# Optimization experiments

Hardware: AMD Instinct MI355X
Metric: run time of the kernel (lower is better)

## Reference

```python
import jax, jax.numpy as jnp
import numpy as np

B = 8192
L = 64
N = L * L          # 4096 lattice sites
H = 256            # hidden size
NL = 8             # coupling layers
NM = N // 2        # masked sites per layer (checkerboard, even L)


def _checkerboard_indices():
    ii, jj = np.meshgrid(np.arange(L), np.arange(L), indexing='ij')
    cb = ((ii + jj) % 2).reshape(-1)
    out = []
    for parity in (0, 1):
        m = np.where(cb == parity)[0].astype(np.int32)   # frozen sites
        u = np.where(cb != parity)[0].astype(np.int32)   # transformed sites
        out.append((jnp.asarray(m), jnp.asarray(u)))
    return out


def setup_inputs() -> dict:
    key = jax.random.key(0)
    ks = jax.random.split(key, 7)
    sc = 0.02  # keep MLP activations in a sane range (orig zero-inits last layer)
    return {
        'z':  jax.random.normal(ks[0], (B, N), dtype=jnp.float32),
        'W1': jax.random.normal(ks[1], (NL, NM, H), dtype=jnp.float32) * sc,
        'b1': jax.random.normal(ks[2], (NL, H), dtype=jnp.float32) * sc,
        'W2': jax.random.normal(ks[3], (NL, H, H), dtype=jnp.float32) * sc,
        'b2': jax.random.normal(ks[4], (NL, H), dtype=jnp.float32) * sc,
        'W3': jax.random.normal(ks[5], (NL, H, 2 * NM), dtype=jnp.float32) * sc,
        'b3': jax.random.normal(ks[6], (NL, 2 * NM), dtype=jnp.float32) * sc,
    }


def reference(z, W1, b1, W2, b2, W3, b3):
    idx = _checkerboard_indices()  # static constants
    x = z
    log_det = jnp.zeros(z.shape[0], dtype=z.dtype)
    for i in range(NL):
        im, iu = idx[i % 2]
        xm = x[:, im]                                        # (B, NM) gather of frozen half
        h = jax.nn.leaky_relu(xm @ W1[i] + b1[i], 0.2)        # (B, H)
        h = jax.nn.leaky_relu(h @ W2[i] + b2[i], 0.2)         # (B, H)
        st = h @ W3[i] + b3[i]                                # (B, 2*NM)
        s, t = jnp.split(st, 2, axis=1)
        s = 2.0 * jnp.tanh(s)
        x = x.at[:, iu].set(x[:, iu] * jnp.exp(s) + t)        # scatter affine-transformed half
        log_det = log_det + s.sum(axis=1)
    return x, log_det
```

## Files before the change

### kernel.cpp

```cpp
#include <hip/hip_runtime.h>
#include <stdint.h>

#define BATCH   8192
#define NTOT    4096
#define HID     256
#define NLAYERS 8
#define NMASK   2048
#define HALF    ((size_t)BATCH * NMASK)

typedef unsigned short ushort_t;
typedef float  f32x4  __attribute__((ext_vector_type(4)));
typedef __bf16 bf16x8 __attribute__((ext_vector_type(8)));
typedef unsigned short u16x4 __attribute__((ext_vector_type(4)));

__device__ __forceinline__ unsigned short f2bf(float f) {
    union { float f; unsigned u; } v; v.f = f;
    unsigned r = v.u + 0x7FFFu + ((v.u >> 16) & 1u);
    return (unsigned short)(r >> 16);
}
__device__ __forceinline__ float bf2f(unsigned short h) {
    union { float f; unsigned u; } v; v.u = ((unsigned)h) << 16;
    return v.f;
}
__device__ __forceinline__ void split2(float f, unsigned short& hi, unsigned short& lo) {
    hi = f2bf(f);
    lo = f2bf(f - bf2f(hi));
}
__device__ __forceinline__ void async16(const void* g, void* l) {
    __builtin_amdgcn_global_load_lds(
        (const __attribute__((address_space(1))) unsigned int*)g,
        (__attribute__((address_space(3))) unsigned int*)l, 16, 0, 0);
}

__global__ __launch_bounds__(256) void split_transpose_kernel(
    const float* __restrict__ W,
    ushort_t* __restrict__ Whi, ushort_t* __restrict__ Wlo,
    int K, int N)
{
    __shared__ float tile[32][33];
    const int l  = blockIdx.z;
    const int k0 = blockIdx.x * 32;
    const int n0 = blockIdx.y * 32;
    const float* Wl = W + (size_t)l * K * N;
    const int tx = threadIdx.x & 31;
    const int ty = threadIdx.x >> 5;
#pragma unroll
    for (int it = 0; it < 4; ++it) {
        int r = ty + it * 8;
        tile[r][tx] = Wl[(size_t)(k0 + r) * N + (n0 + tx)];
    }
    __syncthreads();
    const size_t obase = (size_t)l * N * K;
#pragma unroll
    for (int it = 0; it < 4; ++it) {
        int r = ty + it * 8;
        float v = tile[tx][r];
        unsigned short hi, lo; split2(v, hi, lo);
        size_t oi = obase + (size_t)(n0 + r) * K + (k0 + tx);
        Whi[oi] = hi; Wlo[oi] = lo;
    }
}

__global__ __launch_bounds__(256) void prep_split(
    const float* __restrict__ z,
    ushort_t* __restrict__ xsh, ushort_t* __restrict__ xsl)
{
    size_t f = (((size_t)blockIdx.x * 256) + threadIdx.x) * 4;
    int row = (int)(f >> 11);
    int n   = (int)(f & 2047);
    int sel = (n >> 5) & 1;
    const float4* zp = (const float4*)(z + (size_t)row * NTOT + 2 * (size_t)n);
    float4 z01 = zp[0], z23 = zp[1];
    float e[8] = {z01.x, z01.y, z01.z, z01.w, z23.x, z23.y, z23.z, z23.w};
    u16x4 ah, al, bh, bl;
#pragma unroll
    for (int i = 0; i < 4; ++i) {
        float c0 = e[2 * i], c1 = e[2 * i + 1];
        float a = sel ? c1 : c0;
        float b = sel ? c0 : c1;
        unsigned short h, l;
        split2(a, h, l); ah[i] = h; al[i] = l;
        split2(b, h, l); bh[i] = h; bl[i] = l;
    }
    size_t off = (size_t)row * NMASK + n;
    *(u16x4*)&xsh[off] = ah;        *(u16x4*)&xsl[off] = al;
    *(u16x4*)&xsh[HALF + off] = bh; *(u16x4*)&xsl[HALF + off] = bl;
}

__global__ __launch_bounds__(256) void finalize_x(
    const ushort_t* __restrict__ xsh, const ushort_t* __restrict__ xsl,
    float* __restrict__ xout)
{
    size_t f = (((size_t)blockIdx.x * 256) + threadIdx.x) * 4;
    int row = (int)(f >> 11);
    int n   = (int)(f & 2047);
    int sel = (n >> 5) & 1;
    size_t off = (size_t)row * NMASK + n;
    u16x4 ah = *(const u16x4*)&xsh[off],        al = *(const u16x4*)&xsl[off];
    u16x4 bh = *(const u16x4*)&xsh[HALF + off], bl = *(const u16x4*)&xsl[HALF + off];
    float o[8];
#pragma unroll
    for (int i = 0; i < 4; ++i) {
        float va = bf2f(ah[i]) + bf2f(al[i]);
        float vb = bf2f(bh[i]) + bf2f(bl[i]);
        o[2 * i]     = sel ? vb : va;
        o[2 * i + 1] = sel ? va : vb;
    }
    float* op = xout + (size_t)row * NTOT + 2 * (size_t)n;
    ((float4*)op)[0] = make_float4(o[0], o[1], o[2], o[3]);
    ((float4*)op)[1] = make_float4(o[4], o[5], o[6], o[7]);
}

template<int MODE>
__global__ __launch_bounds__(256) void gemm128(
    const ushort_t* __restrict__ Ahi, const ushort_t* __restrict__ Alo, int lda,
    const ushort_t* __restrict__ Bhi, const ushort_t* __restrict__ Blo, int ldb,
    int nk,
    float* __restrict__ Pout,
    const float* __restrict__ bias,
    ushort_t* __restrict__ Ohi, ushort_t* __restrict__ Olo)
{
    __shared__ __align__(16) ushort_t Ah[128 * 32], Al[128 * 32];
    __shared__ __align__(16) ushort_t Bh[128 * 32], Bl[128 * 32];

    const int t = threadIdx.x;
    const int row0 = blockIdx.x * 128;
    const int col0 = blockIdx.y * 128;
    const int k0   = blockIdx.z * nk * 32;
    const int w  = t >> 6, L = t & 63;
    const int q  = L >> 4, nl = L & 15;
    const int wr = w >> 1, wc = w & 1;

    f32x4 acc[4][4] = {};

    for (int kt = 0; kt < nk; ++kt) {
        const int kk = k0 + kt * 32;
#pragma unroll
        for (int pass = 0; pass < 2; ++pass) {
            const int chunk = t + pass * 256;
            const int r  = chunk >> 2;
            const int ko = (chunk & 3) * 8;
            async16(Ahi + (size_t)(row0 + r) * lda + kk + ko, (char*)Ah + chunk * 16);
            async16(Alo + (size_t)(row0 + r) * lda + kk + ko, (char*)Al + chunk * 16);
            async16(Bhi + (size_t)(col0 + r) * ldb + kk + ko, (char*)Bh + chunk * 16);
            async16(Blo + (size_t)(col0 + r) * ldb + kk + ko, (char*)Bl + chunk * 16);
        }
        __syncthreads();

        bf16x8 a_h[4], a_l[4];
#pragma unroll
        for (int mt = 0; mt < 4; ++mt) {
            const int r = wr * 64 + mt * 16 + nl;
            a_h[mt] = *(const bf16x8*)&Ah[r * 32 + q * 8];
            a_l[mt] = *(const bf16x8*)&Al[r * 32 + q * 8];
        }
#pragma unroll
        for (int nt = 0; nt < 4; ++nt) {
            const int c = wc * 64 + nt * 16 + nl;
            bf16x8 b_h = *(const bf16x8*)&Bh[c * 32 + q * 8];
            bf16x8 b_l = *(const bf16x8*)&Bl[c * 32 + q * 8];
#pragma unroll
            for (int mt = 0; mt < 4; ++mt) {
                acc[mt][nt] = __builtin_amdgcn_mfma_f32_16x16x32_bf16(a_h[mt], b_h, acc[mt][nt], 0, 0, 0);
                acc[mt][nt] = __builtin_amdgcn_mfma_f32_16x16x32_bf16(a_h[mt], b_l, acc[mt][nt], 0, 0, 0);
                acc[mt][nt] = __builtin_amdgcn_mfma_f32_16x16x32_bf16(a_l[mt], b_h, acc[mt][nt], 0, 0, 0);
            }
        }
        __syncthreads();
    }

    if (MODE == 0) {
        float* out = Pout + (size_t)blockIdx.z * BATCH * HID;
#pragma unroll
        for (int mt = 0; mt < 4; ++mt)
#pragma unroll
            for (int r = 0; r < 4; ++r) {
                const int row = row0 + wr * 64 + mt * 16 + q * 4 + r;
                float* op = out + (size_t)row * HID + col0 + wc * 64 + nl;
#pragma unroll
                for (int nt = 0; nt < 4; ++nt)
                    op[nt * 16] = acc[mt][nt][r];
            }
    } else {
#pragma unroll
        for (int mt = 0; mt < 4; ++mt)
#pragma unroll
            for (int nt = 0; nt < 4; ++nt) {
                const int col = col0 + wc * 64 + nt * 16 + nl;
                const float bv = bias[col];
#pragma unroll
                for (int r = 0; r < 4; ++r) {
                    const int row = row0 + wr * 64 + mt * 16 + q * 4 + r;
                    float v = acc[mt][nt][r] + bv;
                    v = v > 0.f ? v : 0.2f * v;
                    unsigned short hh, ll; split2(v, hh, ll);
                    Ohi[(size_t)row * HID + col] = hh;
                    Olo[(size_t)row * HID + col] = ll;
                }
            }
    }
}

__global__ __launch_bounds__(256) void combine_leaky(
    const float* __restrict__ P, const float* __restrict__ bias,
    ushort_t* __restrict__ Ohi, ushort_t* __restrict__ Olo)
{
    size_t f = (((size_t)blockIdx.x * 256) + threadIdx.x) * 4;
    const int col = (int)(f & (HID - 1));
    float4 p0 = *(const float4*)&P[f];
    float4 p1 = *(const float4*)&P[(size_t)BATCH * HID + f];
    float4 bv = *(const float4*)&bias[col];
    float v[4] = {p0.x + p1.x + bv.x, p0.y + p1.y + bv.y,
                  p0.z + p1.z + bv.z, p0.w + p1.w + bv.w};
    u16x4 h, l;
#pragma unroll
    for (int i = 0; i < 4; ++i) {
        float vv = v[i] > 0.f ? v[i] : 0.2f * v[i];
        unsigned short hh, ll; split2(vv, hh, ll);
        h[i] = hh; l[i] = ll;
    }
    *(u16x4*)&Ohi[f] = h;
    *(u16x4*)&Olo[f] = l;
}

__global__ __launch_bounds__(256) void gemm3_update(
    const ushort_t* __restrict__ Ahi, const ushort_t* __restrict__ Alo,
    const ushort_t* __restrict__ Whi, const ushort_t* __restrict__ Wlo,
    const float* __restrict__ b3,
    ushort_t* __restrict__ xsh, ushort_t* __restrict__ xsl,
    float* __restrict__ logdet, int q1)
{
    __shared__ __align__(16) ushort_t Ah[128 * 32], Al[128 * 32];
    __shared__ __align__(16) ushort_t Bsh[64 * 32], Bsl[64 * 32];
    __shared__ __align__(16) ushort_t Bth[64 * 32], Btl[64 * 32];

    const int t = threadIdx.x;
    const int row0 = blockIdx.x * 128;
    const int n0   = blockIdx.y * 64;
    const int w  = t >> 6, L = t & 63;
    const int q  = L >> 4, nl = L & 15;
    const int wr = w >> 1, wc = w & 1;

    f32x4 accS[4][2] = {};
    f32x4 accT[4][2] = {};

    for (int kt = 0; kt < HID / 32; ++kt) {
        const int kk = kt * 32;
#pragma unroll
        for (int pass = 0; pass < 2; ++pass) {
            const int chunk = t + pass * 256;
            const int r  = chunk >> 2;
            const int ko = (chunk & 3) * 8;
            async16(Ahi + (size_t)(row0 + r) * HID + kk + ko, (char*)Ah + chunk * 16);
            async16(Alo + (size_t)(row0 + r) * HID + kk + ko, (char*)Al + chunk * 16);
        }
        {
            const int r  = t >> 2;
            const int ko = (t & 3) * 8;
            const size_t gs = (size_t)(n0 + r) * HID + kk + ko;
            async16(Whi + gs, (char*)Bsh + t * 16);
            async16(Wlo + gs, (char*)Bsl + t * 16);
            async16(Whi + (size_t)NMASK * HID + gs, (char*)Bth + t * 16);
            async16(Wlo + (size_t)NMASK * HID + gs, (char*)Btl + t * 16);
        }
        __syncthreads();

        bf16x8 a_h[4], a_l[4];
#pragma unroll
        for (int mt = 0; mt < 4; ++mt) {
            const int r = wr * 64 + mt * 16 + nl;
            a_h[mt] = *(const bf16x8*)&Ah[r * 32 + q * 8];
            a_l[mt] = *(const bf16x8*)&Al[r * 32 + q * 8];
        }
#pragma unroll
        for (int nt = 0; nt < 2; ++nt) {
            const int c = wc * 32 + nt * 16 + nl;
            bf16x8 bs_h = *(const bf16x8*)&Bsh[c * 32 + q * 8];
            bf16x8 bs_l = *(const bf16x8*)&Bsl[c * 32 + q * 8];
            bf16x8 bt_h = *(const bf16x8*)&Bth[c * 32 + q * 8];
            bf16x8 bt_l = *(const bf16x8*)&Btl[c * 32 + q * 8];
#pragma unroll
            for (int mt = 0; mt < 4; ++mt) {
                accS[mt][nt] = __builtin_amdgcn_mfma_f32_16x16x32_bf16(a_h[mt], bs_h, accS[mt][nt], 0, 0, 0);
                accS[mt][nt] = __builtin_amdgcn_mfma_f32_16x16x32_bf16(a_h[mt], bs_l, accS[mt][nt], 0, 0, 0);
                accS[mt][nt] = __builtin_amdgcn_mfma_f32_16x16x32_bf16(a_l[mt], bs_h, accS[mt][nt], 0, 0, 0);
                accT[mt][nt] = __builtin_amdgcn_mfma_f32_16x16x32_bf16(a_h[mt], bt_h, accT[mt][nt], 0, 0, 0);
                accT[mt][nt] = __builtin_amdgcn_mfma_f32_16x16x32_bf16(a_h[mt], bt_l, accT[mt][nt], 0, 0, 0);
                accT[mt][nt] = __builtin_amdgcn_mfma_f32_16x16x32_bf16(a_l[mt], bt_h, accT[mt][nt], 0, 0, 0);
            }
        }
        __syncthreads();
    }

    ushort_t* xh = xsh + (size_t)q1 * HALF;
    ushort_t* xl = xsl + (size_t)q1 * HALF;
    float ld[4][4] = {};
#pragma unroll
    for (int mt = 0; mt < 4; ++mt) {
#pragma unroll
        for (int nt = 0; nt < 2; ++nt) {
            const int n  = n0 + wc * 32 + nt * 16 + nl;
            const float bs = b3[n];
            const float bt = b3[n + NMASK];
#pragma unroll
            for (int r = 0; r < 4; ++r) {
                const int row = row0 + wr * 64 + mt * 16 + q * 4 + r;
                const float sv = accS[mt][nt][r] + bs;
                const float e2 = __expf(-2.f * fabsf(sv));
                float th = __fdividef(1.f - e2, 1.f + e2);
                th = __builtin_copysignf(th, sv);
                const float s  = 2.f * th;
                const float es = __expf(s);
                const size_t off = (size_t)row * NMASK + n;
                const float old = bf2f(xh[off]) + bf2f(xl[off]);
                const float nv  = old * es + accT[mt][nt][r] + bt;
                unsigned short hh, ll; split2(nv, hh, ll);
                xh[off] = hh; xl[off] = ll;
                ld[mt][r] += s;
            }
        }
    }
#pragma unroll
    for (int mt = 0; mt < 4; ++mt)
#pragma unroll
        for (int r = 0; r < 4; ++r) {
            float v = ld[mt][r];
            v += __shfl_xor(v, 1);
            v += __shfl_xor(v, 2);
            v += __shfl_xor(v, 4);
            v += __shfl_xor(v, 8);
            if (nl == 0)
                atomicAdd(&logdet[row0 + wr * 64 + mt * 16 + q * 4 + r], v);
        }
}

extern "C" void kernel_launch(void* const* d_in, const int* in_sizes, int n_in,
                              void* d_out, int out_size, void* d_ws, size_t ws_size,
                              hipStream_t stream)
{
    const float* z  = (const float*)d_in[0];
    const float* W1 = (const float*)d_in[1];
    const float* b1 = (const float*)d_in[2];
    const float* W2 = (const float*)d_in[3];
    const float* b2 = (const float*)d_in[4];
    const float* W3 = (const float*)d_in[5];
    const float* b3 = (const float*)d_in[6];

    float* xout   = (float*)d_out;
    float* logdet = xout + (size_t)BATCH * NTOT;

    ushort_t* ws = (ushort_t*)d_ws;
    size_t o = 0;
    ushort_t* W1h = ws + o; o += (size_t)NLAYERS * HID * NMASK;
    ushort_t* W1l = ws + o; o += (size_t)NLAYERS * HID * NMASK;
    ushort_t* W2h = ws + o; o += (size_t)NLAYERS * HID * HID;
    ushort_t* W2l = ws + o; o += (size_t)NLAYERS * HID * HID;
    ushort_t* W3h = ws + o; o += (size_t)NLAYERS * NTOT * HID;
    ushort_t* W3l = ws + o; o += (size_t)NLAYERS * NTOT * HID;
    ushort_t* h1h = ws + o; o += (size_t)BATCH * HID;
    ushort_t* h1l = ws + o; o += (size_t)BATCH * HID;
    ushort_t* h2h = ws + o; o += (size_t)BATCH * HID;
    ushort_t* h2l = ws + o; o += (size_t)BATCH * HID;
    ushort_t* xsh = ws + o; o += 2 * HALF;
    ushort_t* xsl = ws + o; o += 2 * HALF;
    float*    P   = (float*)(ws + o);

    hipMemsetAsync(logdet, 0, sizeof(float) * BATCH, stream);

    split_transpose_kernel<<<dim3(NMASK / 32, HID / 32, NLAYERS), 256, 0, stream>>>(
        W1, W1h, W1l, NMASK, HID);
    split_transpose_kernel<<<dim3(HID / 32, HID / 32, NLAYERS), 256, 0, stream>>>(
        W2, W2h, W2l, HID, HID);
    split_transpose_kernel<<<dim3(HID / 32, NTOT / 32, NLAYERS), 256, 0, stream>>>(
        W3, W3h, W3l, HID, NTOT);

    prep_split<<<dim3((unsigned)(HALF / 4 / 256)), 256, 0, stream>>>(z, xsh, xsl);

    for (int i = 0; i < NLAYERS; ++i) {
        const int p  = i & 1;
        const int q1 = 1 - p;
        gemm128<0><<<dim3(BATCH / 128, HID / 128, 2), 256, 0, stream>>>(
            xsh + (size_t)p * HALF, xsl + (size_t)p * HALF, NMASK,
            W1h + (size_t)i * HID * NMASK, W1l + (size_t)i * HID * NMASK, NMASK,
            32, P, nullptr, nullptr, nullptr);
        combine_leaky<<<dim3((unsigned)((size_t)BATCH * HID / 4 / 256)), 256, 0, stream>>>(
            P, b1 + (size_t)i * HID, h1h, h1l);
        gemm128<1><<<dim3(BATCH / 128, HID / 128, 1), 256, 0, stream>>>(
            h1h, h1l, HID,
            W2h + (size_t)i * HID * HID, W2l + (size_t)i * HID * HID, HID,
            8, nullptr, b2 + (size_t)i * HID, h2h, h2l);
        gemm3_update<<<dim3(BATCH / 128, NMASK / 64), 256, 0, stream>>>(
            h2h, h2l,
            W3h + (size_t)i * NTOT * HID, W3l + (size_t)i * NTOT * HID,
            b3 + (size_t)i * NTOT,
            xsh, xsl, logdet, q1);
    }

    finalize_x<<<dim3((unsigned)(HALF / 4 / 256)), 256, 0, stream>>>(xsh, xsl, xout);
}
```

Baseline: 1.799 ms.

## Widen gemm3 tile to 128 columns and split-K 4-way for first two GEMMs

```diff
diff --git a/kernel.cpp b/kernel.cpp
--- a/kernel.cpp
+++ b/kernel.cpp
@@ -111,14 +111,11 @@
     ((float4*)op)[1] = make_float4(o[4], o[5], o[6], o[7]);
 }
 
-template<int MODE>
-__global__ __launch_bounds__(256) void gemm128(
+__global__ __launch_bounds__(256) void gemm_splitk(
     const ushort_t* __restrict__ Ahi, const ushort_t* __restrict__ Alo, int lda,
     const ushort_t* __restrict__ Bhi, const ushort_t* __restrict__ Blo, int ldb,
     int nk,
-    float* __restrict__ Pout,
-    const float* __restrict__ bias,
-    ushort_t* __restrict__ Ohi, ushort_t* __restrict__ Olo)
+    float* __restrict__ Pout)
 {
     __shared__ __align__(16) ushort_t Ah[128 * 32], Al[128 * 32];
     __shared__ __align__(16) ushort_t Bh[128 * 32], Bl[128 * 32];
@@ -169,49 +166,32 @@
         __syncthreads();
     }
 
-    if (MODE == 0) {
-        float* out = Pout + (size_t)blockIdx.z * BATCH * HID;
-#pragma unroll
-        for (int mt = 0; mt < 4; ++mt)
-#pragma unroll
-            for (int r = 0; r < 4; ++r) {
-                const int row = row0 + wr * 64 + mt * 16 + q * 4 + r;
-                float* op = out + (size_t)row * HID + col0 + wc * 64 + nl;
-#pragma unroll
-                for (int nt = 0; nt < 4; ++nt)
-                    op[nt * 16] = acc[mt][nt][r];
-            }
-    } else {
-#pragma unroll
-        for (int mt = 0; mt < 4; ++mt)
-#pragma unroll
-            for (int nt = 0; nt < 4; ++nt) {
-                const int col = col0 + wc * 64 + nt * 16 + nl;
-                const float bv = bias[col];
-#pragma unroll
-                for (int r = 0; r < 4; ++r) {
-                    const int row = row0 + wr * 64 + mt * 16 + q * 4 + r;
-                    float v = acc[mt][nt][r] + bv;
-                    v = v > 0.f ? v : 0.2f * v;
-                    unsigned short hh, ll; split2(v, hh, ll);
-                    Ohi[(size_t)row * HID + col] = hh;
-                    Olo[(size_t)row * HID + col] = ll;
-                }
-            }
-    }
+    float* out = Pout + (size_t)blockIdx.z * BATCH * HID;
+#pragma unroll
+    for (int mt = 0; mt < 4; ++mt)
+#pragma unroll
+        for (int r = 0; r < 4; ++r) {
+            const int row = row0 + wr * 64 + mt * 16 + q * 4 + r;
+            float* op = out + (size_t)row * HID + col0 + wc * 64 + nl;
+#pragma unroll
+            for (int nt = 0; nt < 4; ++nt)
+                op[nt * 16] = acc[mt][nt][r];
+        }
 }
 
 __global__ __launch_bounds__(256) void combine_leaky(
-    const float* __restrict__ P, const float* __restrict__ bias,
+    const float* __restrict__ P, int np, const float* __restrict__ bias,
     ushort_t* __restrict__ Ohi, ushort_t* __restrict__ Olo)
 {
     size_t f = (((size_t)blockIdx.x * 256) + threadIdx.x) * 4;
     const int col = (int)(f & (HID - 1));
-    float4 p0 = *(const float4*)&P[f];
-    float4 p1 = *(const float4*)&P[(size_t)BATCH * HID + f];
+    float4 a = *(const float4*)&P[f];
+    for (int j = 1; j < np; ++j) {
+        float4 p = *(const float4*)&P[(size_t)j * BATCH * HID + f];
+        a.x += p.x; a.y += p.y; a.z += p.z; a.w += p.w;
+    }
     float4 bv = *(const float4*)&bias[col];
-    float v[4] = {p0.x + p1.x + bv.x, p0.y + p1.y + bv.y,
-                  p0.z + p1.z + bv.z, p0.w + p1.w + bv.w};
+    float v[4] = {a.x + bv.x, a.y + bv.y, a.z + bv.z, a.w + bv.w};
     u16x4 h, l;
 #pragma unroll
     for (int i = 0; i < 4; ++i) {
@@ -223,7 +203,7 @@
     *(u16x4*)&Olo[f] = l;
 }
 
-__global__ __launch_bounds__(256) void gemm3_update(
+__global__ __launch_bounds__(256, 2) void gemm3_update(
     const ushort_t* __restrict__ Ahi, const ushort_t* __restrict__ Alo,
     const ushort_t* __restrict__ Whi, const ushort_t* __restrict__ Wlo,
     const float* __restrict__ b3,
@@ -231,18 +211,18 @@
     float* __restrict__ logdet, int q1)
 {
     __shared__ __align__(16) ushort_t Ah[128 * 32], Al[128 * 32];
-    __shared__ __align__(16) ushort_t Bsh[64 * 32], Bsl[64 * 32];
-    __shared__ __align__(16) ushort_t Bth[64 * 32], Btl[64 * 32];
+    __shared__ __align__(16) ushort_t Bsh[128 * 32], Bsl[128 * 32];
+    __shared__ __align__(16) ushort_t Bth[128 * 32], Btl[128 * 32];
 
     const int t = threadIdx.x;
     const int row0 = blockIdx.x * 128;
-    const int n0   = blockIdx.y * 64;
+    const int n0   = blockIdx.y * 128;
     const int w  = t >> 6, L = t & 63;
     const int q  = L >> 4, nl = L & 15;
     const int wr = w >> 1, wc = w & 1;
 
-    f32x4 accS[4][2] = {};
-    f32x4 accT[4][2] = {};
+    f32x4 accS[4][4] = {};
+    f32x4 accT[4][4] = {};
 
     for (int kt = 0; kt < HID / 32; ++kt) {
         const int kk = kt * 32;
@@ -253,15 +233,11 @@
             const int ko = (chunk & 3) * 8;
             async16(Ahi + (size_t)(row0 + r) * HID + kk + ko, (char*)Ah + chunk * 16);
             async16(Alo + (size_t)(row0 + r) * HID + kk + ko, (char*)Al + chunk * 16);
-        }
-        {
-            const int r  = t >> 2;
-            const int ko = (t & 3) * 8;
             const size_t gs = (size_t)(n0 + r) * HID + kk + ko;
-            async16(Whi + gs, (char*)Bsh + t * 16);
-            async16(Wlo + gs, (char*)Bsl + t * 16);
-            async16(Whi + (size_t)NMASK * HID + gs, (char*)Bth + t * 16);
-            async16(Wlo + (size_t)NMASK * HID + gs, (char*)Btl + t * 16);
+            async16(Whi + gs, (char*)Bsh + chunk * 16);
+            async16(Wlo + gs, (char*)Bsl + chunk * 16);
+            async16(Whi + (size_t)NMASK * HID + gs, (char*)Bth + chunk * 16);
+            async16(Wlo + (size_t)NMASK * HID + gs, (char*)Btl + chunk * 16);
         }
         __syncthreads();
 
@@ -273,8 +249,8 @@
             a_l[mt] = *(const bf16x8*)&Al[r * 32 + q * 8];
         }
 #pragma unroll
-        for (int nt = 0; nt < 2; ++nt) {
-            const int c = wc * 32 + nt * 16 + nl;
+        for (int nt = 0; nt < 4; ++nt) {
+            const int c = wc * 64 + nt * 16 + nl;
             bf16x8 bs_h = *(const bf16x8*)&Bsh[c * 32 + q * 8];
             bf16x8 bs_l = *(const bf16x8*)&Bsl[c * 32 + q * 8];
             bf16x8 bt_h = *(const bf16x8*)&Bth[c * 32 + q * 8];
@@ -298,8 +274,8 @@
 #pragma unroll
     for (int mt = 0; mt < 4; ++mt) {
 #pragma unroll
-        for (int nt = 0; nt < 2; ++nt) {
-            const int n  = n0 + wc * 32 + nt * 16 + nl;
+        for (int nt = 0; nt < 4; ++nt) {
+            const int n  = n0 + wc * 64 + nt * 16 + nl;
             const float bs = b3[n];
             const float bt = b3[n + NMASK];
 #pragma unroll
@@ -376,20 +352,21 @@
 
     prep_split<<<dim3((unsigned)(HALF / 4 / 256)), 256, 0, stream>>>(z, xsh, xsl);
 
+    const unsigned cgrid = (unsigned)((size_t)BATCH * HID / 4 / 256);
     for (int i = 0; i < NLAYERS; ++i) {
         const int p  = i & 1;
         const int q1 = 1 - p;
-        gemm128<0><<<dim3(BATCH / 128, HID / 128, 2), 256, 0, stream>>>(
+        gemm_splitk<<<dim3(BATCH / 128, HID / 128, 4), 256, 0, stream>>>(
             xsh + (size_t)p * HALF, xsl + (size_t)p * HALF, NMASK,
             W1h + (size_t)i * HID * NMASK, W1l + (size_t)i * HID * NMASK, NMASK,
-            32, P, nullptr, nullptr, nullptr);
-        combine_leaky<<<dim3((unsigned)((size_t)BATCH * HID / 4 / 256)), 256, 0, stream>>>(
-            P, b1 + (size_t)i * HID, h1h, h1l);
-        gemm128<1><<<dim3(BATCH / 128, HID / 128, 1), 256, 0, stream>>>(
+            16, P);
+        combine_leaky<<<cgrid, 256, 0, stream>>>(P, 4, b1 + (size_t)i * HID, h1h, h1l);
+        gemm_splitk<<<dim3(BATCH / 128, HID / 128, 4), 256, 0, stream>>>(
             h1h, h1l, HID,
             W2h + (size_t)i * HID * HID, W2l + (size_t)i * HID * HID, HID,
-            8, nullptr, b2 + (size_t)i * HID, h2h, h2l);
-        gemm3_update<<<dim3(BATCH / 128, NMASK / 64), 256, 0, stream>>>(
+            2, P);
+        combine_leaky<<<cgrid, 256, 0, stream>>>(P, 4, b2 + (size_t)i * HID, h2h, h2l);
+        gemm3_update<<<dim3(BATCH / 128, NMASK / 128), 256, 0, stream>>>(
             h2h, h2l,
             W3h + (size_t)i * NTOT * HID, W3l + (size_t)i * NTOT * HID,
             b3 + (size_t)i * NTOT,
```

Result: faster. 1.598 ms (-11.2%).
